# Kernel tuning notes

Measured on AMD Instinct MI355X. Metric: run time of the kernel, lower is better.

## Reference

```python
import jax, jax.numpy as jnp
import numpy as np

N_NODES = 100000
N_EDGES = 20000
NNZ = 1600000


def _hconv(x, node_idx, edge_idx, W, b):
    # PyG HypergraphConv (no attention): out = D^-1 H (B^-1 H^T (x W)) + b
    xw = x @ W  # [N, F_out]
    ones = jnp.ones((node_idx.shape[0],), dtype=x.dtype)
    Bdeg = jax.ops.segment_sum(ones, edge_idx, num_segments=N_EDGES)
    Binv = jnp.where(Bdeg > 0, 1.0 / Bdeg, 0.0)
    # node -> hyperedge aggregation
    e = jax.ops.segment_sum(xw[node_idx], edge_idx, num_segments=N_EDGES)
    e = e * Binv[:, None]
    Ddeg = jax.ops.segment_sum(ones, node_idx, num_segments=N_NODES)
    Dinv = jnp.where(Ddeg > 0, 1.0 / Ddeg, 0.0)
    # hyperedge -> node aggregation
    out = jax.ops.segment_sum(e[edge_idx], node_idx, num_segments=N_NODES)
    return out * Dinv[:, None] + b


def setup_inputs() -> dict:
    key = jax.random.key(0)
    ks = jax.random.split(key, 12)
    x = jax.random.normal(ks[0], (N_NODES, 300), dtype=jnp.float32)
    node_idx = jax.random.randint(ks[1], (NNZ,), 0, N_NODES)
    edge_idx = jax.random.randint(ks[2], (NNZ,), 0, N_EDGES)
    hyper_edge_index = jnp.stack([node_idx, edge_idx], axis=0)
    def lin(kw, kb, fi, fo):
        s = 1.0 / np.sqrt(fi)
        W = jax.random.uniform(kw, (fi, fo), jnp.float32, -s, s)
        b = jax.random.uniform(kb, (fo,), jnp.float32, -s, s)
        return W, b
    W1, b1 = lin(ks[3], ks[4], 300, 256)
    W2, b2 = lin(ks[5], ks[6], 256, 256)
    W3, b3 = lin(ks[7], ks[8], 256, 128)
    attn_W, attn_b = lin(ks[9], ks[10], 128, 1)
    return {"x": x, "hyper_edge_index": hyper_edge_index,
            "W1": W1, "b1": b1, "W2": W2, "b2": b2,
            "W3": W3, "b3": b3, "attn_W": attn_W, "attn_b": attn_b}


def reference(x, hyper_edge_index, W1, b1, W2, b2, W3, b3, attn_W, attn_b):
    node_idx = hyper_edge_index[0]
    edge_idx = hyper_edge_index[1]
    h = jax.nn.leaky_relu(_hconv(x, node_idx, edge_idx, W1, b1), negative_slope=0.01)
    # dropout is identity at inference
    h = jax.nn.leaky_relu(_hconv(h, node_idx, edge_idx, W2, b2), negative_slope=0.01)
    h = _hconv(h, node_idx, edge_idx, W3, b3)  # [N, 128]
    # attention pooling over all nodes (softmax along dim 0)
    logits = h @ attn_W + attn_b  # [N, 1]
    attn = jax.nn.softmax(logits, axis=0)
    return jnp.sum(attn * h, axis=0)  # [128]
```

## Files before the change

kernel.cpp:

```cpp
#include <hip/hip_runtime.h>
#include <hip/hip_bf16.h>
#include <string.h>

#define N_NODES 100000
#define N_EDGES 20000
#define NNZ     1600000

#define CHUNK   8192
#define NBE     157
#define NBN     391
#define CAP_E   11264
#define CAP_N   4864
#define NBLK_BIN ((NNZ + CHUNK - 1) / CHUNK)


__device__ __forceinline__ unsigned short f2bf(float f) {
    unsigned int u = __float_as_uint(f);
    unsigned int r = (u + 0x7fffu + ((u >> 16) & 1u)) >> 16;
    return (unsigned short)r;
}
__device__ __forceinline__ float bflo(unsigned int v) { return __uint_as_float(v << 16); }
__device__ __forceinline__ float bfhi(unsigned int v) { return __uint_as_float(v & 0xffff0000u); }
__device__ __forceinline__ unsigned int packbf(float lo, float hi) {
    return ((unsigned int)f2bf(hi) << 16) | (unsigned int)f2bf(lo);
}

__device__ __forceinline__ void async_copy16(const void* g, void* l) {
    __builtin_amdgcn_global_load_lds((const __attribute__((address_space(1))) void*)g,
                                     (__attribute__((address_space(3))) void*)l, 16, 0, 0);
}

typedef __attribute__((ext_vector_type(8))) short bf16x8;
typedef __attribute__((ext_vector_type(4))) float f32x4;
typedef __attribute__((ext_vector_type(4))) unsigned int u32x4;

__device__ __forceinline__ u32x4 ntload4(const void* p) {
    return __builtin_nontemporal_load((const u32x4*)p);
}


__global__ __launch_bounds__(256)
void bin_both(const int* __restrict__ node_idx, const int* __restrict__ edge_idx,
              int* __restrict__ curE, int* __restrict__ curN,
              unsigned int* __restrict__ stagedE, unsigned int* __restrict__ stagedN) {
    __shared__ int hE[NBE], gE[NBE], hN[NBN], gN[NBN];
    int t = threadIdx.x;
    for (int i = t; i < NBE; i += 256) hE[i] = 0;
    for (int i = t; i < NBN; i += 256) hN[i] = 0;
    __syncthreads();
    long base = (long)blockIdx.x * CHUNK;
    for (int k = 0; k < CHUNK / 256; k++) {
        long i = base + t + k * 256;
        if (i < NNZ) {
            atomicAdd(&hE[edge_idx[i] >> 7], 1);
            atomicAdd(&hN[node_idx[i] >> 8], 1);
        }
    }
    __syncthreads();
    for (int i = t; i < NBE; i += 256) gE[i] = hE[i] ? atomicAdd(&curE[i], hE[i]) : 0;
    for (int i = t; i < NBN; i += 256) gN[i] = hN[i] ? atomicAdd(&curN[i], hN[i]) : 0;
    __syncthreads();
    for (int i = t; i < NBE; i += 256) hE[i] = 0;
    for (int i = t; i < NBN; i += 256) hN[i] = 0;
    __syncthreads();
    for (int k = 0; k < CHUNK / 256; k++) {
        long i = base + t + k * 256;
        if (i < NNZ) {
            int e = edge_idx[i], n = node_idx[i];
            int be = e >> 7, bn = n >> 8;
            int pe = gE[be] + atomicAdd(&hE[be], 1);
            if (pe < CAP_E) stagedE[(size_t)be * CAP_E + pe] = ((unsigned)e << 17) | (unsigned)n;
            int pn = gN[bn] + atomicAdd(&hN[bn], 1);
            if (pn < CAP_N) stagedN[(size_t)bn * CAP_N + pn] = ((unsigned)n << 15) | (unsigned)e;
        }
    }
}

__global__ __launch_bounds__(256)
void build_csr2(const unsigned int* __restrict__ staged, const int* __restrict__ cnts,
                int cap, int kshift, int bshift, int nkey,
                int* __restrict__ off, int* __restrict__ endv,
                float* __restrict__ inv, int* __restrict__ csr) {
    __shared__ int cnt[256];
    __shared__ int cur[256];
    int b = blockIdx.x, t = threadIdx.x;
    int kpb = 1 << bshift;
    int key0 = b << bshift;
    unsigned int vmask = (1u << kshift) - 1u;
    int s = b * cap;
    int n = min(cnts[b], cap);
    if (t < kpb) cnt[t] = 0;
    __syncthreads();
    for (int j = t; j < n; j += 256)
        atomicAdd(&cnt[(int)(staged[s + j] >> kshift) - key0], 1);
    __syncthreads();
    int v = (t < kpb) ? cnt[t] : 0;
    cur[t] = v; __syncthreads();
    for (int st = 1; st < 256; st <<= 1) {
        int x = (t >= st) ? cur[t - st] : 0;
        __syncthreads();
        cur[t] += x;
        __syncthreads();
    }
    int excl = cur[t] - v;
    __syncthreads();
    if (t < kpb) {
        int key = key0 + t;
        if (key < nkey) {
            off[key] = s + excl;
            endv[key] = s + excl + v;
            inv[key] = (v > 0) ? 1.0f / (float)v : 0.0f;
        }
        cur[t] = excl;
    }
    __syncthreads();
    for (int j = t; j < n; j += 256) {
        unsigned int pk = staged[s + j];
        int k = (int)(pk >> kshift) - key0;
        int pos = s + atomicAdd(&cur[k], 1);
        csr[pos] = (int)(pk & vmask);
    }
}


__global__ __launch_bounds__(256)
void convert_pad_x_v(const float* __restrict__ x, unsigned short* __restrict__ xb) {
    int t = threadIdx.x;
    if (t >= 240) return;
    int c = t % 40;
    int r = blockIdx.x * 6 + t / 40;
    if (r >= N_NODES) return;
    const float* xr = x + (size_t)r * 300 + c * 8;
    uint4 ov;
    if (c < 37) {
        float4 a = ((const float4*)xr)[0];
        float4 b = ((const float4*)xr)[1];
        ov.x = packbf(a.x, a.y); ov.y = packbf(a.z, a.w);
        ov.z = packbf(b.x, b.y); ov.w = packbf(b.z, b.w);
    } else if (c == 37) {
        float4 a = ((const float4*)xr)[0];
        ov.x = packbf(a.x, a.y); ov.y = packbf(a.z, a.w);
        ov.z = 0u; ov.w = 0u;
    } else {
        ov.x = ov.y = ov.z = ov.w = 0u;
    }
    *(uint4*)(xb + (size_t)r * 320 + c * 8) = ov;
}

__global__ void transpose_all(const float* __restrict__ W1, const float* __restrict__ W2,
                              const float* __restrict__ W3,
                              unsigned short* __restrict__ Wt1, unsigned short* __restrict__ Wt2,
                              unsigned short* __restrict__ Wt3) {
    int b = blockIdx.x;
    int t = threadIdx.x;
    if (b < 256) {
        for (int k = t; k < 320; k += 256)
            Wt1[(size_t)b * 320 + k] = (k < 300) ? f2bf(W1[(size_t)k * 256 + b]) : (unsigned short)0;
    } else if (b < 512) {
        int n = b - 256;
        Wt2[(size_t)n * 256 + t] = f2bf(W2[(size_t)t * 256 + n]);
    } else {
        int n = b - 512;
        Wt3[(size_t)n * 256 + t] = f2bf(W3[(size_t)t * 128 + n]);
    }
}


__global__ __launch_bounds__(256)
void gemm_bf16(const unsigned short* __restrict__ A,
               const unsigned short* __restrict__ Bt,
               unsigned short* __restrict__ C,
               int M, int Kp, int N) {
    __shared__ unsigned short As[128 * 32];
    __shared__ unsigned short Bs[128 * 32];
    int tid = threadIdx.x;
    int lane = tid & 63;
    int w = tid >> 6;
    int row0 = blockIdx.x * 128;
    int col0 = blockIdx.y * 128;
    int wm = w & 1, wn = w >> 1;

    f32x4 acc[4][4];
    #pragma unroll
    for (int i = 0; i < 4; i++)
        #pragma unroll
        for (int j = 0; j < 4; j++) acc[i][j] = (f32x4){0.f, 0.f, 0.f, 0.f};

    int sr = lane >> 2;
    int sc = lane & 3;

    for (int k0 = 0; k0 < Kp; k0 += 32) {
        #pragma unroll
        for (int c = 0; c < 2; c++) {
            int r = w * 32 + c * 16 + sr;
            int gr = row0 + r; if (gr >= M) gr = M - 1;
            const unsigned short* g = A + (size_t)gr * Kp + k0 + sc * 8;
            async_copy16(g, (void*)(As + (w * 32 + c * 16) * 32));
        }
        #pragma unroll
        for (int c = 0; c < 2; c++) {
            int r = w * 32 + c * 16 + sr;
            const unsigned short* g = Bt + (size_t)(col0 + r) * Kp + k0 + sc * 8;
            async_copy16(g, (void*)(Bs + (w * 32 + c * 16) * 32));
        }
        __syncthreads();

        bf16x8 a[4], b[4];
        #pragma unroll
        for (int i = 0; i < 4; i++)
            a[i] = *(const bf16x8*)(As + (wm * 64 + i * 16 + (lane & 15)) * 32 + (lane >> 4) * 8);
        #pragma unroll
        for (int j = 0; j < 4; j++)
            b[j] = *(const bf16x8*)(Bs + (wn * 64 + j * 16 + (lane & 15)) * 32 + (lane >> 4) * 8);
        #pragma unroll
        for (int i = 0; i < 4; i++)
            #pragma unroll
            for (int j = 0; j < 4; j++)
                acc[i][j] = __builtin_amdgcn_mfma_f32_16x16x32_bf16(a[i], b[j], acc[i][j], 0, 0, 0);
        __syncthreads();
    }

    int crow = (lane >> 4) * 4;
    int ccol = lane & 15;
    #pragma unroll
    for (int i = 0; i < 4; i++)
        #pragma unroll
        for (int r = 0; r < 4; r++) {
            int gr = row0 + wm * 64 + i * 16 + crow + r;
            if (gr < M) {
                #pragma unroll
                for (int j = 0; j < 4; j++) {
                    int gc = col0 + wn * 64 + j * 16 + ccol;
                    C[(size_t)gr * N + gc] = f2bf(acc[i][j][r]);
                }
            }
        }
}


#define ACC8(v)  { a[0] += bflo((v).x); a[1] += bfhi((v).x); \
                   a[2] += bflo((v).y); a[3] += bfhi((v).y); \
                   a[4] += bflo((v).z); a[5] += bfhi((v).z); \
                   a[6] += bflo((v).w); a[7] += bfhi((v).w); }

__global__ __launch_bounds__(256)
void edge_agg256(const unsigned short* __restrict__ X, const int* __restrict__ off,
                 const int* __restrict__ endv, const int* __restrict__ csr,
                 const float* __restrict__ inv, unsigned short* __restrict__ E) {
    int wv = threadIdx.x >> 6, lane = threadIdx.x & 63;
    int seg = blockIdx.x * 4 + wv;
    if (seg >= N_EDGES) return;
    int s = off[seg], t = endv[seg];
    int half = lane >> 5, l32 = lane & 31;
    const char* Xc = (const char*)X;
    unsigned lo = (unsigned)l32 << 4;
    float a[8] = {0.f, 0.f, 0.f, 0.f, 0.f, 0.f, 0.f, 0.f};
    int j = s;
    for (; j + 12 <= t; j += 12) {
        unsigned o[6];
        #pragma unroll
        for (int q = 0; q < 6; q++) o[q] = ((unsigned)csr[j + 2 * q + half] << 9) + lo;
        uint4 v[6];
        #pragma unroll
        for (int q = 0; q < 6; q++) v[q] = *(const uint4*)(Xc + o[q]);
        __builtin_amdgcn_sched_barrier(0);
        #pragma unroll
        for (int q = 0; q < 6; q++) ACC8(v[q]);
    }
    for (; j + 1 < t; j += 2) {
        uint4 v = *(const uint4*)(Xc + (((unsigned)csr[j + half] << 9) + lo));
        ACC8(v);
    }
    if (j < t && half == 0) {
        uint4 v = *(const uint4*)(Xc + (((unsigned)csr[j] << 9) + lo));
        ACC8(v);
    }
    #pragma unroll
    for (int k = 0; k < 8; k++) a[k] += __shfl_down(a[k], 32);
    if (half == 0) {
        float bi = inv[seg];
        uint4 o;
        o.x = packbf(a[0] * bi, a[1] * bi); o.y = packbf(a[2] * bi, a[3] * bi);
        o.z = packbf(a[4] * bi, a[5] * bi); o.w = packbf(a[6] * bi, a[7] * bi);
        ((uint4*)E)[(size_t)seg * 32 + l32] = o;
    }
}

__global__ __launch_bounds__(256)
void edge_agg256_nt(const unsigned short* __restrict__ X, const int* __restrict__ off,
                    const int* __restrict__ endv, const int* __restrict__ csr,
                    const float* __restrict__ inv, unsigned short* __restrict__ E) {
    int wv = threadIdx.x >> 6, lane = threadIdx.x & 63;
    int seg = blockIdx.x * 4 + wv;
    if (seg >= N_EDGES) return;
    int s = off[seg], t = endv[seg];
    int half = lane >> 5, l32 = lane & 31;
    const char* Xc = (const char*)X;
    unsigned lo = (unsigned)l32 << 4;
    float a[8] = {0.f, 0.f, 0.f, 0.f, 0.f, 0.f, 0.f, 0.f};
    int j = s;
    for (; j + 12 <= t; j += 12) {
        unsigned o[6];
        #pragma unroll
        for (int q = 0; q < 6; q++) o[q] = ((unsigned)csr[j + 2 * q + half] << 9) + lo;
        u32x4 v[6];
        #pragma unroll
        for (int q = 0; q < 6; q++) v[q] = ntload4(Xc + o[q]);
        __builtin_amdgcn_sched_barrier(0);
        #pragma unroll
        for (int q = 0; q < 6; q++) ACC8(v[q]);
    }
    for (; j + 1 < t; j += 2) {
        u32x4 v = ntload4(Xc + (((unsigned)csr[j + half] << 9) + lo));
        ACC8(v);
    }
    if (j < t && half == 0) {
        u32x4 v = ntload4(Xc + (((unsigned)csr[j] << 9) + lo));
        ACC8(v);
    }
    #pragma unroll
    for (int k = 0; k < 8; k++) a[k] += __shfl_down(a[k], 32);
    if (half == 0) {
        float bi = inv[seg];
        uint4 o;
        o.x = packbf(a[0] * bi, a[1] * bi); o.y = packbf(a[2] * bi, a[3] * bi);
        o.z = packbf(a[4] * bi, a[5] * bi); o.w = packbf(a[6] * bi, a[7] * bi);
        ((uint4*)E)[(size_t)seg * 32 + l32] = o;
    }
}

__global__ __launch_bounds__(256)
void node_agg256(const unsigned short* __restrict__ Eb, const int* __restrict__ off,
                 const int* __restrict__ endv, const int* __restrict__ csr,
                 const float* __restrict__ inv, const float* __restrict__ bias,
                 unsigned short* __restrict__ outB) {
    int wv = threadIdx.x >> 6, lane = threadIdx.x & 63;
    int seg = blockIdx.x * 4 + wv;
    if (seg >= N_NODES) return;
    int s = off[seg], t = endv[seg];
    int half = lane >> 5, l32 = lane & 31;
    const char* Ec = (const char*)Eb;
    unsigned lo = (unsigned)l32 << 4;
    float a[8] = {0.f, 0.f, 0.f, 0.f, 0.f, 0.f, 0.f, 0.f};
    int j = s;
    for (; j + 12 <= t; j += 12) {
        unsigned o[6];
        #pragma unroll
        for (int q = 0; q < 6; q++) o[q] = ((unsigned)csr[j + 2 * q + half] << 9) + lo;
        uint4 v[6];
        #pragma unroll
        for (int q = 0; q < 6; q++) v[q] = *(const uint4*)(Ec + o[q]);
        __builtin_amdgcn_sched_barrier(0);
        #pragma unroll
        for (int q = 0; q < 6; q++) ACC8(v[q]);
    }
    for (; j + 1 < t; j += 2) {
        uint4 v = *(const uint4*)(Ec + (((unsigned)csr[j + half] << 9) + lo));
        ACC8(v);
    }
    if (j < t && half == 0) {
        uint4 v = *(const uint4*)(Ec + (((unsigned)csr[j] << 9) + lo));
        ACC8(v);
    }
    #pragma unroll
    for (int k = 0; k < 8; k++) a[k] += __shfl_down(a[k], 32);
    if (half == 0) {
        float di = inv[seg];
        float4 b0 = ((const float4*)bias)[l32 * 2];
        float4 b1 = ((const float4*)bias)[l32 * 2 + 1];
        float o0 = a[0] * di + b0.x, o1 = a[1] * di + b0.y;
        float o2 = a[2] * di + b0.z, o3 = a[3] * di + b0.w;
        float o4 = a[4] * di + b1.x, o5 = a[5] * di + b1.y;
        float o6 = a[6] * di + b1.z, o7 = a[7] * di + b1.w;
        o0 = (o0 > 0.f) ? o0 : 0.01f * o0;  o1 = (o1 > 0.f) ? o1 : 0.01f * o1;
        o2 = (o2 > 0.f) ? o2 : 0.01f * o2;  o3 = (o3 > 0.f) ? o3 : 0.01f * o3;
        o4 = (o4 > 0.f) ? o4 : 0.01f * o4;  o5 = (o5 > 0.f) ? o5 : 0.01f * o5;
        o6 = (o6 > 0.f) ? o6 : 0.01f * o6;  o7 = (o7 > 0.f) ? o7 : 0.01f * o7;
        uint4 o;
        o.x = packbf(o0, o1); o.y = packbf(o2, o3);
        o.z = packbf(o4, o5); o.w = packbf(o6, o7);
        ((uint4*)outB)[(size_t)seg * 32 + l32] = o;
    }
}

__global__ __launch_bounds__(256)
void node_agg128f(const unsigned short* __restrict__ Eb, const int* __restrict__ off,
                  const int* __restrict__ endv, const int* __restrict__ csr,
                  const float* __restrict__ inv, const float* __restrict__ bias,
                  float* __restrict__ outF) {
    int wv = threadIdx.x >> 6, lane = threadIdx.x & 63;
    int seg = blockIdx.x * 4 + wv;
    if (seg >= N_NODES) return;
    int s = off[seg], t = endv[seg];
    int quad = lane >> 4, l16 = lane & 15;
    const char* Ec = (const char*)Eb;
    unsigned lo = (unsigned)l16 << 4;
    float a[8] = {0.f, 0.f, 0.f, 0.f, 0.f, 0.f, 0.f, 0.f};
    int j = s;
    for (; j + 16 <= t; j += 16) {
        unsigned o[4];
        #pragma unroll
        for (int q = 0; q < 4; q++) o[q] = ((unsigned)csr[j + 4 * q + quad] << 8) + lo;
        uint4 v[4];
        #pragma unroll
        for (int q = 0; q < 4; q++) v[q] = *(const uint4*)(Ec + o[q]);
        __builtin_amdgcn_sched_barrier(0);
        #pragma unroll
        for (int q = 0; q < 4; q++) ACC8(v[q]);
    }
    for (; j + 4 <= t; j += 4) {
        uint4 v = *(const uint4*)(Ec + (((unsigned)csr[j + quad] << 8) + lo));
        ACC8(v);
    }
    if (j < t && j + quad < t) {
        uint4 v = *(const uint4*)(Ec + (((unsigned)csr[j + quad] << 8) + lo));
        ACC8(v);
    }
    #pragma unroll
    for (int k = 0; k < 8; k++) {
        a[k] += __shfl_down(a[k], 32);
        a[k] += __shfl_down(a[k], 16);
    }
    if (lane < 16) {
        float di = inv[seg];
        float4 b0 = ((const float4*)bias)[l16 * 2];
        float4 b1 = ((const float4*)bias)[l16 * 2 + 1];
        float4 o0 = make_float4(a[0] * di + b0.x, a[1] * di + b0.y,
                                a[2] * di + b0.z, a[3] * di + b0.w);
        float4 o1 = make_float4(a[4] * di + b1.x, a[5] * di + b1.y,
                                a[6] * di + b1.z, a[7] * di + b1.w);
        ((float4*)outF)[(size_t)seg * 32 + l16 * 2]     = o0;
        ((float4*)outF)[(size_t)seg * 32 + l16 * 2 + 1] = o1;
    }
}


__global__ __launch_bounds__(256)
void logits_kernel(const float* __restrict__ H, const float* __restrict__ aW,
                   const float* __restrict__ aB, float* __restrict__ logits,
                   float* __restrict__ pmax, int N) {
    int lane = threadIdx.x & 63;
    int wave = threadIdx.x >> 6;
    int waveGlobal = blockIdx.x * 4 + wave;
    int stride = gridDim.x * 4;
    float2 w2 = ((const float2*)aW)[lane];
    float lmax = -1e30f;
    float ab = aB[0];
    for (int n = waveGlobal; n < N; n += stride) {
        float2 h2 = ((const float2*)(H + (size_t)n * 128))[lane];
        float d = h2.x * w2.x + h2.y * w2.y;
        #pragma unroll
        for (int s = 32; s > 0; s >>= 1) d += __shfl_xor(d, s, 64);
        float lg = d + ab;
        if (lane == 0) logits[n] = lg;
        lmax = fmaxf(lmax, lg);
    }
    __shared__ float wmax[4];
    if (lane == 0) wmax[wave] = lmax;
    __syncthreads();
    if (threadIdx.x == 0) {
        float m = fmaxf(fmaxf(wmax[0], wmax[1]), fmaxf(wmax[2], wmax[3]));
        pmax[blockIdx.x] = m;
    }
}

__global__ __launch_bounds__(128)
void weighted_sum(const float* __restrict__ H, const float* __restrict__ logits,
                  const float* __restrict__ pmax, float* __restrict__ gacc,
                  float* __restrict__ gsum, int N) {
    int f = threadIdx.x;
    __shared__ float smax[2];
    float m = -1e30f;
    for (int i = f; i < 400; i += 128) m = fmaxf(m, pmax[i]);
    #pragma unroll
    for (int s = 32; s > 0; s >>= 1) m = fmaxf(m, __shfl_xor(m, s, 64));
    if ((f & 63) == 0) smax[f >> 6] = m;
    __syncthreads();
    float mx = fmaxf(smax[0], smax[1]);
    float acc = 0.f, ls = 0.f;
    for (int n = blockIdx.x; n < N; n += gridDim.x) {
        float w = __expf(logits[n] - mx);
        acc += w * H[(size_t)n * 128 + f];
        if (f == 0) ls += w;
    }
    atomicAdd(&gacc[f], acc);
    if (f == 0) atomicAdd(gsum, ls);
}

__global__ __launch_bounds__(128)
void finalize(const float* __restrict__ gacc, const float* __restrict__ gsum,
              float* __restrict__ out) {
    int f = threadIdx.x;
    out[f] = gacc[f] / gsum[0];
}


extern "C" void kernel_launch(void* const* d_in, const int* in_sizes, int n_in,
                              void* d_out, int out_size, void* d_ws, size_t ws_size,
                              hipStream_t stream) {
    const float* x        = (const float*)d_in[0];
    const int*   node_idx = (const int*)d_in[1];
    const int*   edge_idx = node_idx + NNZ;
    const float* W1 = (const float*)d_in[2];
    const float* b1 = (const float*)d_in[3];
    const float* W2 = (const float*)d_in[4];
    const float* b2 = (const float*)d_in[5];
    const float* W3 = (const float*)d_in[6];
    const float* b3 = (const float*)d_in[7];
    const float* aW = (const float*)d_in[8];
    const float* aB = (const float*)d_in[9];
    float* out = (float*)d_out;

    char* ws = (char*)d_ws;
    size_t off = 0;
    auto take = [&](size_t bytes) -> char* {
        char* r = ws + off;
        off = (off + bytes + 255) & ~(size_t)255;
        return r;
    };

    char* cur_base = take((size_t)(NBE + NBN) * 4);
    int* curE = (int*)cur_base;
    int* curN = curE + NBE;
    int*   offE = (int*)take((size_t)N_EDGES * 4);
    int*   endE = (int*)take((size_t)N_EDGES * 4);
    int*   offN = (int*)take((size_t)N_NODES * 4);
    int*   endN = (int*)take((size_t)N_NODES * 4);
    float* Binv = (float*)take((size_t)N_EDGES * 4);
    float* Dinv = (float*)take((size_t)N_NODES * 4);
    int*   csrE = (int*)take((size_t)NBE * CAP_E * 4);
    int*   csrN = (int*)take((size_t)NBN * CAP_N * 4);

    unsigned short* xb  = (unsigned short*)take((size_t)N_NODES * 320 * 2);
    unsigned short* Wt1 = (unsigned short*)take((size_t)256 * 320 * 2);
    unsigned short* Wt2 = (unsigned short*)take((size_t)256 * 256 * 2);
    unsigned short* Wt3 = (unsigned short*)take((size_t)128 * 256 * 2);
    unsigned short* xw   = (unsigned short*)take((size_t)N_NODES * 256 * 2);
    unsigned short* hb   = (unsigned short*)take((size_t)N_NODES * 256 * 2);
    unsigned short* eagg = (unsigned short*)take((size_t)N_EDGES * 256 * 2);
    unsigned short* eb   = (unsigned short*)take((size_t)N_EDGES * 256 * 2);
    float* h3 = (float*)xb;

    unsigned int* stagedE = (unsigned int*)xw;
    unsigned int* stagedN = stagedE + (size_t)NBE * CAP_E;

    float* logits = (float*)take((size_t)N_NODES * 4);
    float* pmax   = (float*)take(400 * 4);
    char* acc_base = take((128 + 1) * 4);
    float* gacc = (float*)acc_base;
    float* gsum = gacc + 128;

    hipMemsetAsync(cur_base, 0, (size_t)(NBE + NBN) * 4, stream);
    hipMemsetAsync(acc_base, 0, (128 + 1) * 4, stream);

    bin_both<<<NBLK_BIN, 256, 0, stream>>>(node_idx, edge_idx, curE, curN, stagedE, stagedN);
    build_csr2<<<NBE, 256, 0, stream>>>(stagedE, curE, CAP_E, 17, 7, N_EDGES, offE, endE, Binv, csrE);
    build_csr2<<<NBN, 256, 0, stream>>>(stagedN, curN, CAP_N, 15, 8, N_NODES, offN, endN, Dinv, csrN);

    convert_pad_x_v<<<(N_NODES + 5) / 6, 256, 0, stream>>>(x, xb);
    transpose_all<<<640, 256, 0, stream>>>(W1, W2, W3, Wt1, Wt2, Wt3);

    const int MB = (N_NODES + 127) / 128;
    const int ME = (N_EDGES + 127) / 128;
    const int EB = N_EDGES / 4;
    const int NB = N_NODES / 4;

    gemm_bf16<<<dim3(MB, 2), 256, 0, stream>>>(xb, Wt1, xw, N_NODES, 320, 256);
    edge_agg256<<<EB, 256, 0, stream>>>(xw, offE, endE, csrE, Binv, eb);
    node_agg256<<<NB, 256, 0, stream>>>(eb, offN, endN, csrN, Dinv, b1, hb);

    edge_agg256_nt<<<EB, 256, 0, stream>>>(hb, offE, endE, csrE, Binv, eagg);
    gemm_bf16<<<dim3(ME, 2), 256, 0, stream>>>(eagg, Wt2, eb, N_EDGES, 256, 256);
    node_agg256<<<NB, 256, 0, stream>>>(eb, offN, endN, csrN, Dinv, b2, hb);

    edge_agg256<<<EB, 256, 0, stream>>>(hb, offE, endE, csrE, Binv, eagg);
    gemm_bf16<<<dim3(ME, 1), 256, 0, stream>>>(eagg, Wt3, eb, N_EDGES, 256, 128);
    node_agg128f<<<NB, 256, 0, stream>>>(eb, offN, endN, csrN, Dinv, b3, h3);

    logits_kernel<<<400, 256, 0, stream>>>(h3, aW, aB, logits, pmax, N_NODES);
    weighted_sum<<<512, 128, 0, stream>>>(h3, logits, pmax, gacc, gsum, N_NODES);
    finalize<<<1, 128, 0, stream>>>(gacc, gsum, out);
}
```

Measured before the change: 1.036 ms.

## Reorder layer-3 GEMM before edge aggregation to gather 128-wide rows

For the third layer, the linear transform now runs on all nodes first (N×256→128) and the edge aggregation then gathers 128-wide bf16 rows through a new edge_agg128 kernel, where each quarter-wave handles one incidence. Before, 256-wide rows were gathered and the GEMM ran on the smaller edge matrix. This halves the bytes gathered over the 1.6M incidences, but the GEMM now covers 100k rows instead of 20k. The layer-2 edge aggregation also drops nontemporal loads and goes back to the regular edge_agg256 kernel.

```diff
diff --git a/kernel.cpp b/kernel.cpp
--- a/kernel.cpp
+++ b/kernel.cpp
@@ -32,11 +32,6 @@
 
 typedef __attribute__((ext_vector_type(8))) short bf16x8;
 typedef __attribute__((ext_vector_type(4))) float f32x4;
-typedef __attribute__((ext_vector_type(4))) unsigned int u32x4;
-
-__device__ __forceinline__ u32x4 ntload4(const void* p) {
-    return __builtin_nontemporal_load((const u32x4*)p);
-}
 
 
 __global__ __launch_bounds__(256)
@@ -287,45 +282,48 @@
 }
 
 __global__ __launch_bounds__(256)
-void edge_agg256_nt(const unsigned short* __restrict__ X, const int* __restrict__ off,
-                    const int* __restrict__ endv, const int* __restrict__ csr,
-                    const float* __restrict__ inv, unsigned short* __restrict__ E) {
+void edge_agg128(const unsigned short* __restrict__ X, const int* __restrict__ off,
+                 const int* __restrict__ endv, const int* __restrict__ csr,
+                 const float* __restrict__ inv, unsigned short* __restrict__ E) {
     int wv = threadIdx.x >> 6, lane = threadIdx.x & 63;
     int seg = blockIdx.x * 4 + wv;
     if (seg >= N_EDGES) return;
     int s = off[seg], t = endv[seg];
-    int half = lane >> 5, l32 = lane & 31;
+    int quad = lane >> 4, l16 = lane & 15;
     const char* Xc = (const char*)X;
-    unsigned lo = (unsigned)l32 << 4;
+    unsigned lo = (unsigned)l16 << 4;
     float a[8] = {0.f, 0.f, 0.f, 0.f, 0.f, 0.f, 0.f, 0.f};
     int j = s;
-    for (; j + 12 <= t; j += 12) {
-        unsigned o[6];
-        #pragma unroll
-        for (int q = 0; q < 6; q++) o[q] = ((unsigned)csr[j + 2 * q + half] << 9) + lo;
-        u32x4 v[6];
-        #pragma unroll
-        for (int q = 0; q < 6; q++) v[q] = ntload4(Xc + o[q]);
+    for (; j + 16 <= t; j += 16) {
+        unsigned o[4];
+        #pragma unroll
+        for (int q = 0; q < 4; q++) o[q] = ((unsigned)csr[j + 4 * q + quad] << 8) + lo;
+        uint4 v[4];
+        #pragma unroll
+        for (int q = 0; q < 4; q++) v[q] = *(const uint4*)(Xc + o[q]);
         __builtin_amdgcn_sched_barrier(0);
         #pragma unroll
-        for (int q = 0; q < 6; q++) ACC8(v[q]);
-    }
-    for (; j + 1 < t; j += 2) {
-        u32x4 v = ntload4(Xc + (((unsigned)csr[j + half] << 9) + lo));
-        ACC8(v);
-    }
-    if (j < t && half == 0) {
-        u32x4 v = ntload4(Xc + (((unsigned)csr[j] << 9) + lo));
-        ACC8(v);
-    }
-    #pragma unroll
-    for (int k = 0; k < 8; k++) a[k] += __shfl_down(a[k], 32);
-    if (half == 0) {
+        for (int q = 0; q < 4; q++) ACC8(v[q]);
+    }
+    for (; j + 4 <= t; j += 4) {
+        uint4 v = *(const uint4*)(Xc + (((unsigned)csr[j + quad] << 8) + lo));
+        ACC8(v);
+    }
+    if (j < t && j + quad < t) {
+        uint4 v = *(const uint4*)(Xc + (((unsigned)csr[j + quad] << 8) + lo));
+        ACC8(v);
+    }
+    #pragma unroll
+    for (int k = 0; k < 8; k++) {
+        a[k] += __shfl_down(a[k], 32);
+        a[k] += __shfl_down(a[k], 16);
+    }
+    if (lane < 16) {
         float bi = inv[seg];
         uint4 o;
         o.x = packbf(a[0] * bi, a[1] * bi); o.y = packbf(a[2] * bi, a[3] * bi);
         o.z = packbf(a[4] * bi, a[5] * bi); o.w = packbf(a[6] * bi, a[7] * bi);
-        ((uint4*)E)[(size_t)seg * 32 + l32] = o;
+        *(uint4*)((char*)E + (size_t)seg * 256 + lo) = o;
     }
 }
 
@@ -569,12 +567,12 @@
     edge_agg256<<<EB, 256, 0, stream>>>(xw, offE, endE, csrE, Binv, eb);
     node_agg256<<<NB, 256, 0, stream>>>(eb, offN, endN, csrN, Dinv, b1, hb);
 
-    edge_agg256_nt<<<EB, 256, 0, stream>>>(hb, offE, endE, csrE, Binv, eagg);
+    edge_agg256<<<EB, 256, 0, stream>>>(hb, offE, endE, csrE, Binv, eagg);
     gemm_bf16<<<dim3(ME, 2), 256, 0, stream>>>(eagg, Wt2, eb, N_EDGES, 256, 256);
     node_agg256<<<NB, 256, 0, stream>>>(eb, offN, endN, csrN, Dinv, b2, hb);
 
-    edge_agg256<<<EB, 256, 0, stream>>>(hb, offE, endE, csrE, Binv, eagg);
-    gemm_bf16<<<dim3(ME, 1), 256, 0, stream>>>(eagg, Wt3, eb, N_EDGES, 256, 128);
+    gemm_bf16<<<dim3(MB, 1), 256, 0, stream>>>(hb, Wt3, xw, N_NODES, 256, 128);
+    edge_agg128<<<EB, 256, 0, stream>>>(xw, offE, endE, csrE, Binv, eb);
     node_agg128f<<<NB, 256, 0, stream>>>(eb, offN, endN, csrN, Dinv, b3, h3);
 
     logits_kernel<<<400, 256, 0, stream>>>(h3, aW, aB, logits, pmax, N_NODES);
```

Result: faster. 967.6 us (-6.6%).
